# Kernel optimization log

Hardware: AMD Instinct MI355X
Metric: run time of the kernel (lower is better)

Reference implementation:

```python
import jax, jax.numpy as jnp
import numpy as np

H = 768
NH = 12
DH = H // NH  # 64
EPS = 1e-6


def _split_heads(x):
    # [B,S,H] -> [B,NH,S,DH]
    B, S, _ = x.shape
    return x.reshape(B, S, NH, DH).transpose(0, 2, 1, 3)


def setup_inputs() -> dict:
    key = jax.random.key(0)
    ks = jax.random.split(key, 16)
    B, S = 4, 1024
    sc = 0.02
    return {
        "hidden_states": jax.random.normal(ks[0], (B, S, H), jnp.float32),
        "time_embeddings": jax.random.normal(ks[1], (B, S, H), jnp.float32),
        "space_embeddings": jax.random.normal(ks[2], (B, S, H), jnp.float32),
        "attention_mask": jnp.zeros((B, 1, 1, S), jnp.float32),
        "Wq": jax.random.normal(ks[3], (H, H), jnp.float32) * sc,
        "bq": jnp.zeros((H,), jnp.float32),
        "Wk": jax.random.normal(ks[4], (H, H), jnp.float32) * sc,
        "bk": jnp.zeros((H,), jnp.float32),
        "Wv": jax.random.normal(ks[5], (H, H), jnp.float32) * sc,
        "bv": jnp.zeros((H,), jnp.float32),
        "Wt": jax.random.normal(ks[6], (H, H), jnp.float32) * sc,
        "bt": jnp.zeros((H,), jnp.float32),
        "Ws": jax.random.normal(ks[7], (H, H), jnp.float32) * sc,
        "bs": jnp.zeros((H,), jnp.float32),
    }


def reference(hidden_states, time_embeddings, space_embeddings, attention_mask,
              Wq, bq, Wk, bk, Wv, bv, Wt, bt, Ws, bs):
    q = _split_heads(hidden_states @ Wq.T + bq)   # [B,NH,S,DH]
    k = _split_heads(hidden_states @ Wk.T + bk)
    v = _split_heads(hidden_states @ Wv.T + bv)
    T = _split_heads(time_embeddings @ Wt.T + bt)
    Sp = _split_heads(space_embeddings @ Ws.T + bs)

    base = jnp.einsum("bhqd,bhkd->bhqk", q, k)
    T_norm = jnp.linalg.norm(T, axis=-1, keepdims=True)          # [B,NH,S,1]
    time_sim = jnp.einsum("bhqd,bhkd->bhqk", T, T) / (T_norm + EPS)
    S_norm = jnp.linalg.norm(Sp, axis=-1, keepdims=True)
    space_sim = jnp.einsum("bhqd,bhkd->bhqk", Sp, Sp) / (S_norm + EPS)

    scores = base * time_sim * space_sim / jnp.sqrt(jnp.float32(DH))
    scores = scores + attention_mask
    probs = jax.nn.softmax(scores, axis=-1)  # dropout is identity in eval
    ctx = jnp.einsum("bhqk,bhkd->bhqd", probs, v)
    B, _, S, _ = ctx.shape
    return ctx.transpose(0, 2, 1, 3).reshape(B, S, H)
```

## Files before the change

### kernel.cpp

```cpp
#include <hip/hip_runtime.h>

#define NHEADS 12
#define SEQ    1024
#define HDIM   768
#define DHEAD  64
#define BH_TOT 48
#define EPSN   1e-6f

typedef __attribute__((ext_vector_type(8))) short    bf8;
typedef __attribute__((ext_vector_type(4))) float    fx4;
typedef __attribute__((ext_vector_type(4))) _Float16 h4;

#define SZT 3145728u
#define WSZ 589824u

__device__ __forceinline__ float bf2f(unsigned short h) {
  union { unsigned int u; float f; } v; v.u = ((unsigned int)h) << 16; return v.f;
}
__device__ __forceinline__ unsigned short f2bf(float f) {
  union { float f; unsigned int u; } v; v.f = f;
  unsigned int u = v.u;
  return (unsigned short)((u + 0x7FFFu + ((u >> 16) & 1u)) >> 16);
}

typedef __attribute__((address_space(3))) unsigned int lds_u32;
typedef __attribute__((address_space(1))) const unsigned int glb_u32;
__device__ __forceinline__ void gld16(const unsigned short* g, unsigned short* l) {
  __builtin_amdgcn_global_load_lds((glb_u32*)g, (lds_u32*)l, 16, 0, 0);
}

__global__ void convert_kernel(const float* __restrict__ hs, const float* __restrict__ te,
                               const float* __restrict__ se,
                               const float* __restrict__ Wq, const float* __restrict__ Wk,
                               const float* __restrict__ Wv, const float* __restrict__ Wt,
                               const float* __restrict__ Ws2,
                               unsigned short* __restrict__ ws)
{
  const int z = blockIdx.y;
  const float* src;
  unsigned short* dst;
  int n;
  if (z < 3) {
    src = (z == 0) ? hs : (z == 1) ? te : se;
    dst = ws + (size_t)(5 + z) * SZT;
    n = 3145728;
  } else {
    src = (z == 3) ? Wq : (z == 4) ? Wk : (z == 5) ? Wv : (z == 6) ? Wt : Ws2;
    dst = ws + (size_t)8 * SZT + (size_t)(z - 3) * WSZ;
    n = 589824;
  }
  const int base = (blockIdx.x * 256 + threadIdx.x) * 8;
  if (base >= n) return;
  const fx4 a = *(const fx4*)(src + base);
  const fx4 b = *(const fx4*)(src + base + 4);
  bf8 o;
#pragma unroll
  for (int j = 0; j < 4; ++j) { o[j] = (short)f2bf(a[j]); o[4 + j] = (short)f2bf(b[j]); }
  *(bf8*)(dst + base) = o;
}

__global__ __launch_bounds__(256, 3)
void proj_kernel(unsigned short* __restrict__ ws,
                 const float* __restrict__ bq, const float* __restrict__ bk,
                 const float* __restrict__ bv, const float* __restrict__ bt,
                 const float* __restrict__ bs)
{
  __shared__ unsigned short Xs[2][4096];
  __shared__ unsigned short Ys[2][4096];

  const int z = blockIdx.z;
  const unsigned short* X = ws + (size_t)5 * SZT + (size_t)((z < 3) ? 0 : (z - 2)) * SZT;
  const unsigned short* W = ws + (size_t)8 * SZT + (size_t)z * WSZ;
  const float* bias = (z == 0) ? bq : (z == 1) ? bk : (z == 2) ? bv : (z == 3) ? bt : bs;
  unsigned short* out = ws + (size_t)((z < 2) ? z : (z == 2) ? 4 : (z == 3) ? 2 : 3) * SZT;

  const int tid   = threadIdx.x;
  const int lane  = tid & 63;
  const int wid   = tid >> 6;
  const int wm    = wid >> 1, wn = wid & 1;
  const int colid = lane & 15, quad = lane >> 4;
  const int m0 = blockIdx.y * 128, n0 = blockIdx.x * 128;

  auto stage = [&](int kt, int pb) {
#pragma unroll
    for (int i = 0; i < 2; ++i) {
      const int slot = i * 256 + tid;
      const int row = slot >> 2, ch = slot & 3;
      gld16(X + (m0 + row) * HDIM + kt + ch * 8, &Xs[pb][slot * 8]);
      gld16(W + (n0 + row) * HDIM + kt + ch * 8, &Ys[pb][slot * 8]);
    }
  };

  fx4 acc[4][4];
#pragma unroll
  for (int i = 0; i < 4; ++i)
#pragma unroll
    for (int j = 0; j < 4; ++j) acc[i][j] = (fx4){0.f, 0.f, 0.f, 0.f};

  stage(0, 0);
  __syncthreads();

  for (int it = 0; it < 24; ++it) {
    const int pb = it & 1;
    if (it + 1 < 24) stage((it + 1) * 32, pb ^ 1);

    bf8 af[4], bfr[4];
#pragma unroll
    for (int i = 0; i < 4; ++i)
      af[i] = *(const bf8*)&Xs[pb][(wm * 64 + i * 16 + colid) * 32 + quad * 8];
#pragma unroll
    for (int j = 0; j < 4; ++j)
      bfr[j] = *(const bf8*)&Ys[pb][(wn * 64 + j * 16 + colid) * 32 + quad * 8];
#pragma unroll
    for (int i = 0; i < 4; ++i)
#pragma unroll
      for (int j = 0; j < 4; ++j)
        acc[i][j] = __builtin_amdgcn_mfma_f32_16x16x32_bf16(af[i], bfr[j], acc[i][j], 0, 0, 0);
    __syncthreads();
  }

  if (z != 2) {
#pragma unroll
    for (int i = 0; i < 4; ++i) {
      const int r0 = m0 + wm * 64 + i * 16 + quad * 4;
      const int bb = r0 >> 10, s0 = r0 & 1023;
#pragma unroll
      for (int j = 0; j < 4; ++j) {
        const int c = n0 + wn * 64 + j * 16 + colid;
        const int h = c >> 6, d = c & 63;
        const float bvl = bias[c];
        unsigned short* op = out + (((bb * NHEADS + h) * SEQ + s0) * DHEAD + d);
#pragma unroll
        for (int reg = 0; reg < 4; ++reg)
          op[reg * DHEAD] = f2bf(acc[i][j][reg] + bvl);
      }
    }
  } else {
#pragma unroll
    for (int i = 0; i < 4; ++i) {
      const int r0 = m0 + wm * 64 + i * 16 + quad * 4;
      const int bb = r0 >> 10, s0 = r0 & 1023;
#pragma unroll
      for (int j = 0; j < 4; ++j) {
        const int c = n0 + wn * 64 + j * 16 + colid;
        const int h = c >> 6, d = c & 63;
        const float bvl = bias[c];
        h4 pk;
#pragma unroll
        for (int reg = 0; reg < 4; ++reg)
          pk[reg] = (_Float16)(acc[i][j][reg] + bvl);
        *(h4*)(void*)(out + ((size_t)((bb * NHEADS + h) * DHEAD + d)) * SEQ + s0) = pk;
      }
    }
  }
}

__global__ __launch_bounds__(256, 2)
void attn_kernel(const unsigned short* __restrict__ ws,
                 const float* __restrict__ maskb,
                 float* __restrict__ outb)
{
  const unsigned short* Qb  = ws;
  const unsigned short* GT0 = ws + (size_t)1 * SZT;
  const unsigned short* GT1 = ws + (size_t)2 * SZT;
  const unsigned short* GT2 = ws + (size_t)3 * SZT;
  const unsigned short* Vtu = ws + (size_t)4 * SZT;

  __shared__ unsigned short Ls[2][4][64][64];

  const int tid   = threadIdx.x;
  const int lane  = tid & 63;
  const int wid   = tid >> 6;
  const int colid = lane & 15, quad = lane >> 4;

  const int lin = blockIdx.x;
  const int xcd = lin & 7;
  const int idx = lin >> 3;
  const int bh  = xcd * 6 + (idx % 6);
  const int qx  = idx / 6;
  const int b   = bh / NHEADS, h = bh % NHEADS;
  const int q0  = qx * 128 + wid * 32;
  const int base_h = bh * SEQ * DHEAD;

  bf8 bqf[2][2], btf[2][2], bsf[2][2];
  float rs[2];
#pragma unroll
  for (int g = 0; g < 2; ++g) {
    const int row = q0 + g * 16 + colid;
    const unsigned short* qp = Qb  + base_h + row * 64 + quad * 8;
    const unsigned short* tp = GT1 + base_h + row * 64 + quad * 8;
    const unsigned short* sp = GT2 + base_h + row * 64 + quad * 8;
    bqf[g][0] = *(const bf8*)qp;  bqf[g][1] = *(const bf8*)(qp + 32);
    btf[g][0] = *(const bf8*)tp;  btf[g][1] = *(const bf8*)(tp + 32);
    bsf[g][0] = *(const bf8*)sp;  bsf[g][1] = *(const bf8*)(sp + 32);
    float t2 = 0.f, s2 = 0.f;
#pragma unroll
    for (int fr = 0; fr < 2; ++fr)
#pragma unroll
      for (int j = 0; j < 8; ++j) {
        const float tv = bf2f((unsigned short)btf[g][fr][j]);
        const float sv2 = bf2f((unsigned short)bsf[g][fr][j]);
        t2 += tv * tv; s2 += sv2 * sv2;
      }
    t2 += __shfl_xor(t2, 16); t2 += __shfl_xor(t2, 32);
    s2 += __shfl_xor(s2, 16); s2 += __shfl_xor(s2, 32);
    rs[g] = 1.0f / ((sqrtf(t2) + EPSN) * (sqrtf(s2) + EPSN) * 8.0f);
  }

  auto stage = [&](int kb, int pb) {
#pragma unroll
    for (int i = 0; i < 8; ++i) {
      const int s  = i * 256 + tid;
      const int r  = (s >> 3) & 63;
      const int cs = ((s & 7) ^ (r & 7)) * 8;
      unsigned short* dst = &Ls[pb][0][0][0] + s * 8;
      if (i < 2)      gld16(GT0 + base_h + (kb + r) * 64 + cs, dst);
      else if (i < 4) gld16(GT1 + base_h + (kb + r) * 64 + cs, dst);
      else if (i < 6) gld16(GT2 + base_h + (kb + r) * 64 + cs, dst);
      else            gld16(Vtu + ((size_t)(bh * 64 + r)) * 1024 + kb + cs, dst);
    }
  };

  float m_[2], l_[2];
  fx4 o[2][4];
#pragma unroll
  for (int g = 0; g < 2; ++g) {
    m_[g] = -1.0e30f; l_[g] = 0.f;
#pragma unroll
    for (int fd = 0; fd < 4; ++fd) o[g][fd] = (fx4){0.f, 0.f, 0.f, 0.f};
  }
  const fx4 zero = (fx4){0.f, 0.f, 0.f, 0.f};

  stage(0, 0);
  __syncthreads();

#pragma unroll 1
  for (int t = 0; t < 16; ++t) {
    const int pb = t & 1;
    if (t + 1 < 16) stage((t + 1) * 64, pb ^ 1);
    const int kb = t * 64;

#pragma unroll
    for (int hh = 0; hh < 2; ++hh) {
      bf8 ak[2][2], at_[2][2], as_[2][2];
      h4 vv[2][4];
      fx4 mk[2];
#pragma unroll
      for (int ff = 0; ff < 2; ++ff) {
        const int f   = hh * 2 + ff;
        const int row = f * 16 + colid;
        const int sw  = row & 7;
#pragma unroll
        for (int fr = 0; fr < 2; ++fr) {
          const int co = ((quad + fr * 4) ^ sw) * 8;
          ak[ff][fr]  = *(const bf8*)&Ls[pb][0][row][co];
          at_[ff][fr] = *(const bf8*)&Ls[pb][1][row][co];
          as_[ff][fr] = *(const bf8*)&Ls[pb][2][row][co];
        }
#pragma unroll
        for (int fd = 0; fd < 4; ++fd) {
          const int vr = fd * 16 + colid;
          const int vo = (((f * 2 + (quad >> 1)) ^ (vr & 7)) * 8) + (quad & 1) * 4;
          vv[ff][fd] = *(const h4*)&Ls[pb][3][vr][vo];
        }
        mk[ff] = *(const fx4*)(maskb + b * SEQ + kb + f * 16 + quad * 4);
      }

#pragma unroll
      for (int g = 0; g < 2; ++g) {
        float sv[2][4];
#pragma unroll
        for (int ff = 0; ff < 2; ++ff) {
          fx4 ab = __builtin_amdgcn_mfma_f32_16x16x32_bf16(ak[ff][0], bqf[g][0], zero, 0, 0, 0);
          ab = __builtin_amdgcn_mfma_f32_16x16x32_bf16(ak[ff][1], bqf[g][1], ab, 0, 0, 0);
          fx4 tt = __builtin_amdgcn_mfma_f32_16x16x32_bf16(at_[ff][0], btf[g][0], zero, 0, 0, 0);
          tt = __builtin_amdgcn_mfma_f32_16x16x32_bf16(at_[ff][1], btf[g][1], tt, 0, 0, 0);
          fx4 ss = __builtin_amdgcn_mfma_f32_16x16x32_bf16(as_[ff][0], bsf[g][0], zero, 0, 0, 0);
          ss = __builtin_amdgcn_mfma_f32_16x16x32_bf16(as_[ff][1], bsf[g][1], ss, 0, 0, 0);
#pragma unroll
          for (int reg = 0; reg < 4; ++reg)
            sv[ff][reg] = (ab[reg] * tt[reg]) * ss[reg] * rs[g] + mk[ff][reg];
        }

        float bm = sv[0][0];
#pragma unroll
        for (int ff = 0; ff < 2; ++ff)
#pragma unroll
          for (int reg = 0; reg < 4; ++reg) bm = fmaxf(bm, sv[ff][reg]);
        bm = fmaxf(bm, __shfl_xor(bm, 16));
        bm = fmaxf(bm, __shfl_xor(bm, 32));
        const float mn = fmaxf(m_[g], bm);
        const float alpha = __expf(m_[g] - mn);
        float rsum = 0.f;
        h4 pa[2];
#pragma unroll
        for (int ff = 0; ff < 2; ++ff)
#pragma unroll
          for (int reg = 0; reg < 4; ++reg) {
            const float p = __expf(sv[ff][reg] - mn);
            rsum += p;
            pa[ff][reg] = (_Float16)p;
          }
        rsum += __shfl_xor(rsum, 16);
        rsum += __shfl_xor(rsum, 32);
        l_[g] = l_[g] * alpha + rsum;
        m_[g] = mn;

        float ar[4];
#pragma unroll
        for (int reg = 0; reg < 4; ++reg) ar[reg] = __shfl(alpha, quad * 4 + reg);
#pragma unroll
        for (int fd = 0; fd < 4; ++fd)
#pragma unroll
          for (int reg = 0; reg < 4; ++reg) o[g][fd][reg] *= ar[reg];

#pragma unroll
        for (int ff = 0; ff < 2; ++ff)
#pragma unroll
          for (int fd = 0; fd < 4; ++fd)
            o[g][fd] = __builtin_amdgcn_mfma_f32_16x16x16f16(pa[ff], vv[ff][fd], o[g][fd], 0, 0, 0);
      }
    }
    __syncthreads();
  }

#pragma unroll
  for (int g = 0; g < 2; ++g) {
    const float linv = 1.0f / l_[g];
    float ir[4];
#pragma unroll
    for (int reg = 0; reg < 4; ++reg) ir[reg] = __shfl(linv, quad * 4 + reg);
#pragma unroll
    for (int reg = 0; reg < 4; ++reg) {
      const int s = q0 + g * 16 + quad * 4 + reg;
#pragma unroll
      for (int fd = 0; fd < 4; ++fd)
        outb[(size_t)(b * SEQ + s) * HDIM + h * DHEAD + fd * 16 + colid] = o[g][fd][reg] * ir[reg];
    }
  }
}

extern "C" void kernel_launch(void* const* d_in, const int* in_sizes, int n_in,
                              void* d_out, int out_size, void* d_ws, size_t ws_size,
                              hipStream_t stream)
{
  (void)in_sizes; (void)n_in; (void)out_size; (void)ws_size;
  const float* hs   = (const float*)d_in[0];
  const float* te   = (const float*)d_in[1];
  const float* se   = (const float*)d_in[2];
  const float* mask = (const float*)d_in[3];
  const float* Wq   = (const float*)d_in[4];
  const float* bq   = (const float*)d_in[5];
  const float* Wk   = (const float*)d_in[6];
  const float* bk   = (const float*)d_in[7];
  const float* Wv   = (const float*)d_in[8];
  const float* bv   = (const float*)d_in[9];
  const float* Wt   = (const float*)d_in[10];
  const float* bt   = (const float*)d_in[11];
  const float* Wsp  = (const float*)d_in[12];
  const float* bsp  = (const float*)d_in[13];
  float* out = (float*)d_out;
  unsigned short* ws = (unsigned short*)d_ws;

  convert_kernel<<<dim3(1536, 8), 256, 0, stream>>>(hs, te, se, Wq, Wk, Wv, Wt, Wsp, ws);
  proj_kernel<<<dim3(6, 32, 5), 256, 0, stream>>>(ws, bq, bk, bv, bt, bsp);
  attn_kernel<<<dim3(384), 256, 0, stream>>>(ws, mask, out);
}
```

Before: 202.7 us.

## Halve query rows per block, double grid, read V directly from global

The attention kernel now processes 16 query rows per wave (64 per block) instead of 32, so the grid doubles to 768 blocks. V is no longer staged through LDS; each wave loads its V fragments straight from global memory, which shrinks shared memory to three K/T/S tiles and raises the launch-bounds occupancy target to 3 blocks per CU. The goal is better CU fill and more latency hiding. The cost is that each K/T/S tile staged in LDS is reused by half as many query rows, and the uncached global V reads add latency inside the inner loop.

```diff
diff --git a/kernel.cpp b/kernel.cpp
--- a/kernel.cpp
+++ b/kernel.cpp
@@ -155,7 +155,7 @@
   }
 }
 
-__global__ __launch_bounds__(256, 2)
+__global__ __launch_bounds__(256, 3)
 void attn_kernel(const unsigned short* __restrict__ ws,
                  const float* __restrict__ maskb,
                  float* __restrict__ outb)
@@ -164,9 +164,9 @@
   const unsigned short* GT0 = ws + (size_t)1 * SZT;
   const unsigned short* GT1 = ws + (size_t)2 * SZT;
   const unsigned short* GT2 = ws + (size_t)3 * SZT;
-  const unsigned short* Vtu = ws + (size_t)4 * SZT;
-
-  __shared__ unsigned short Ls[2][4][64][64];
+  const _Float16* Vtf = (const _Float16*)(ws + (size_t)4 * SZT);
+
+  __shared__ unsigned short Ls[2][3][64][64];
 
   const int tid   = threadIdx.x;
   const int lane  = tid & 63;
@@ -179,56 +179,50 @@
   const int bh  = xcd * 6 + (idx % 6);
   const int qx  = idx / 6;
   const int b   = bh / NHEADS, h = bh % NHEADS;
-  const int q0  = qx * 128 + wid * 32;
+  const int q0  = qx * 64 + wid * 16;
   const int base_h = bh * SEQ * DHEAD;
 
-  bf8 bqf[2][2], btf[2][2], bsf[2][2];
-  float rs[2];
-#pragma unroll
-  for (int g = 0; g < 2; ++g) {
-    const int row = q0 + g * 16 + colid;
+  bf8 bqf[2], btf[2], bsf[2];
+  float rs;
+  {
+    const int row = q0 + colid;
     const unsigned short* qp = Qb  + base_h + row * 64 + quad * 8;
     const unsigned short* tp = GT1 + base_h + row * 64 + quad * 8;
     const unsigned short* sp = GT2 + base_h + row * 64 + quad * 8;
-    bqf[g][0] = *(const bf8*)qp;  bqf[g][1] = *(const bf8*)(qp + 32);
-    btf[g][0] = *(const bf8*)tp;  btf[g][1] = *(const bf8*)(tp + 32);
-    bsf[g][0] = *(const bf8*)sp;  bsf[g][1] = *(const bf8*)(sp + 32);
+    bqf[0] = *(const bf8*)qp;  bqf[1] = *(const bf8*)(qp + 32);
+    btf[0] = *(const bf8*)tp;  btf[1] = *(const bf8*)(tp + 32);
+    bsf[0] = *(const bf8*)sp;  bsf[1] = *(const bf8*)(sp + 32);
     float t2 = 0.f, s2 = 0.f;
 #pragma unroll
     for (int fr = 0; fr < 2; ++fr)
 #pragma unroll
       for (int j = 0; j < 8; ++j) {
-        const float tv = bf2f((unsigned short)btf[g][fr][j]);
-        const float sv2 = bf2f((unsigned short)bsf[g][fr][j]);
+        const float tv = bf2f((unsigned short)btf[fr][j]);
+        const float sv2 = bf2f((unsigned short)bsf[fr][j]);
         t2 += tv * tv; s2 += sv2 * sv2;
       }
     t2 += __shfl_xor(t2, 16); t2 += __shfl_xor(t2, 32);
     s2 += __shfl_xor(s2, 16); s2 += __shfl_xor(s2, 32);
-    rs[g] = 1.0f / ((sqrtf(t2) + EPSN) * (sqrtf(s2) + EPSN) * 8.0f);
+    rs = 1.0f / ((sqrtf(t2) + EPSN) * (sqrtf(s2) + EPSN) * 8.0f);
   }
 
   auto stage = [&](int kb, int pb) {
 #pragma unroll
-    for (int i = 0; i < 8; ++i) {
+    for (int i = 0; i < 6; ++i) {
       const int s  = i * 256 + tid;
       const int r  = (s >> 3) & 63;
       const int cs = ((s & 7) ^ (r & 7)) * 8;
       unsigned short* dst = &Ls[pb][0][0][0] + s * 8;
       if (i < 2)      gld16(GT0 + base_h + (kb + r) * 64 + cs, dst);
       else if (i < 4) gld16(GT1 + base_h + (kb + r) * 64 + cs, dst);
-      else if (i < 6) gld16(GT2 + base_h + (kb + r) * 64 + cs, dst);
-      else            gld16(Vtu + ((size_t)(bh * 64 + r)) * 1024 + kb + cs, dst);
+      else            gld16(GT2 + base_h + (kb + r) * 64 + cs, dst);
     }
   };
 
-  float m_[2], l_[2];
-  fx4 o[2][4];
-#pragma unroll
-  for (int g = 0; g < 2; ++g) {
-    m_[g] = -1.0e30f; l_[g] = 0.f;
-#pragma unroll
-    for (int fd = 0; fd < 4; ++fd) o[g][fd] = (fx4){0.f, 0.f, 0.f, 0.f};
-  }
+  float m_ = -1.0e30f, l_ = 0.f;
+  fx4 o[4];
+#pragma unroll
+  for (int fd = 0; fd < 4; ++fd) o[fd] = (fx4){0.f, 0.f, 0.f, 0.f};
   const fx4 zero = (fx4){0.f, 0.f, 0.f, 0.f};
 
   stage(0, 0);
@@ -258,84 +252,78 @@
           as_[ff][fr] = *(const bf8*)&Ls[pb][2][row][co];
         }
 #pragma unroll
-        for (int fd = 0; fd < 4; ++fd) {
-          const int vr = fd * 16 + colid;
-          const int vo = (((f * 2 + (quad >> 1)) ^ (vr & 7)) * 8) + (quad & 1) * 4;
-          vv[ff][fd] = *(const h4*)&Ls[pb][3][vr][vo];
+        for (int fd = 0; fd < 4; ++fd)
+          vv[ff][fd] = *(const h4*)(Vtf + (size_t)(bh * DHEAD + fd * 16 + colid) * SEQ
+                                        + kb + f * 16 + quad * 4);
+        mk[ff] = *(const fx4*)(maskb + b * SEQ + kb + f * 16 + quad * 4);
+      }
+
+      float sv[2][4];
+#pragma unroll
+      for (int ff = 0; ff < 2; ++ff) {
+        fx4 ab = __builtin_amdgcn_mfma_f32_16x16x32_bf16(ak[ff][0], bqf[0], zero, 0, 0, 0);
+        ab = __builtin_amdgcn_mfma_f32_16x16x32_bf16(ak[ff][1], bqf[1], ab, 0, 0, 0);
+        fx4 tt = __builtin_amdgcn_mfma_f32_16x16x32_bf16(at_[ff][0], btf[0], zero, 0, 0, 0);
+        tt = __builtin_amdgcn_mfma_f32_16x16x32_bf16(at_[ff][1], btf[1], tt, 0, 0, 0);
+        fx4 ss = __builtin_amdgcn_mfma_f32_16x16x32_bf16(as_[ff][0], bsf[0], zero, 0, 0, 0);
+        ss = __builtin_amdgcn_mfma_f32_16x16x32_bf16(as_[ff][1], bsf[1], ss, 0, 0, 0);
+#pragma unroll
+        for (int reg = 0; reg < 4; ++reg)
+          sv[ff][reg] = (ab[reg] * tt[reg]) * ss[reg] * rs + mk[ff][reg];
+      }
+
+      float bm = sv[0][0];
+#pragma unroll
+      for (int ff = 0; ff < 2; ++ff)
+#pragma unroll
+        for (int reg = 0; reg < 4; ++reg) bm = fmaxf(bm, sv[ff][reg]);
+      bm = fmaxf(bm, __shfl_xor(bm, 16));
+      bm = fmaxf(bm, __shfl_xor(bm, 32));
+      const float mn = fmaxf(m_, bm);
+      const float alpha = __expf(m_ - mn);
+      float rsum = 0.f;
+      h4 pa[2];
+#pragma unroll
+      for (int ff = 0; ff < 2; ++ff)
+#pragma unroll
+        for (int reg = 0; reg < 4; ++reg) {
+          const float p = __expf(sv[ff][reg] - mn);
+          rsum += p;
+          pa[ff][reg] = (_Float16)p;
         }
-        mk[ff] = *(const fx4*)(maskb + b * SEQ + kb + f * 16 + quad * 4);
-      }
-
-#pragma unroll
-      for (int g = 0; g < 2; ++g) {
-        float sv[2][4];
-#pragma unroll
-        for (int ff = 0; ff < 2; ++ff) {
-          fx4 ab = __builtin_amdgcn_mfma_f32_16x16x32_bf16(ak[ff][0], bqf[g][0], zero, 0, 0, 0);
-          ab = __builtin_amdgcn_mfma_f32_16x16x32_bf16(ak[ff][1], bqf[g][1], ab, 0, 0, 0);
-          fx4 tt = __builtin_amdgcn_mfma_f32_16x16x32_bf16(at_[ff][0], btf[g][0], zero, 0, 0, 0);
-          tt = __builtin_amdgcn_mfma_f32_16x16x32_bf16(at_[ff][1], btf[g][1], tt, 0, 0, 0);
-          fx4 ss = __builtin_amdgcn_mfma_f32_16x16x32_bf16(as_[ff][0], bsf[g][0], zero, 0, 0, 0);
-          ss = __builtin_amdgcn_mfma_f32_16x16x32_bf16(as_[ff][1], bsf[g][1], ss, 0, 0, 0);
-#pragma unroll
-          for (int reg = 0; reg < 4; ++reg)
-            sv[ff][reg] = (ab[reg] * tt[reg]) * ss[reg] * rs[g] + mk[ff][reg];
-        }
-
-        float bm = sv[0][0];
-#pragma unroll
-        for (int ff = 0; ff < 2; ++ff)
-#pragma unroll
-          for (int reg = 0; reg < 4; ++reg) bm = fmaxf(bm, sv[ff][reg]);
-        bm = fmaxf(bm, __shfl_xor(bm, 16));
-        bm = fmaxf(bm, __shfl_xor(bm, 32));
-        const float mn = fmaxf(m_[g], bm);
-        const float alpha = __expf(m_[g] - mn);
-        float rsum = 0.f;
-        h4 pa[2];
-#pragma unroll
-        for (int ff = 0; ff < 2; ++ff)
-#pragma unroll
-          for (int reg = 0; reg < 4; ++reg) {
-            const float p = __expf(sv[ff][reg] - mn);
-            rsum += p;
-            pa[ff][reg] = (_Float16)p;
-          }
-        rsum += __shfl_xor(rsum, 16);
-        rsum += __shfl_xor(rsum, 32);
-        l_[g] = l_[g] * alpha + rsum;
-        m_[g] = mn;
-
-        float ar[4];
-#pragma unroll
-        for (int reg = 0; reg < 4; ++reg) ar[reg] = __shfl(alpha, quad * 4 + reg);
+      rsum += __shfl_xor(rsum, 16);
+      rsum += __shfl_xor(rsum, 32);
+      l_ = l_ * alpha + rsum;
+      m_ = mn;
+
+      float ar[4];
+#pragma unroll
+      for (int reg = 0; reg < 4; ++reg) ar[reg] = __shfl(alpha, quad * 4 + reg);
+#pragma unroll
+      for (int fd = 0; fd < 4; ++fd)
+#pragma unroll
+        for (int reg = 0; reg < 4; ++reg) o[fd][reg] *= ar[reg];
+
+#pragma unroll
+      for (int ff = 0; ff < 2; ++ff)
 #pragma unroll
         for (int fd = 0; fd < 4; ++fd)
-#pragma unroll
-          for (int reg = 0; reg < 4; ++reg) o[g][fd][reg] *= ar[reg];
-
-#pragma unroll
-        for (int ff = 0; ff < 2; ++ff)
-#pragma unroll
-          for (int fd = 0; fd < 4; ++fd)
-            o[g][fd] = __builtin_amdgcn_mfma_f32_16x16x16f16(pa[ff], vv[ff][fd], o[g][fd], 0, 0, 0);
-      }
+          o[fd] = __builtin_amdgcn_mfma_f32_16x16x16f16(pa[ff], vv[ff][fd], o[fd], 0, 0, 0);
     }
     __syncthreads();
   }
 
-#pragma unroll
-  for (int g = 0; g < 2; ++g) {
-    const float linv = 1.0f / l_[g];
+  {
+    const float linv = 1.0f / l_;
     float ir[4];
 #pragma unroll
     for (int reg = 0; reg < 4; ++reg) ir[reg] = __shfl(linv, quad * 4 + reg);
 #pragma unroll
     for (int reg = 0; reg < 4; ++reg) {
-      const int s = q0 + g * 16 + quad * 4 + reg;
+      const int s = q0 + quad * 4 + reg;
 #pragma unroll
       for (int fd = 0; fd < 4; ++fd)
-        outb[(size_t)(b * SEQ + s) * HDIM + h * DHEAD + fd * 16 + colid] = o[g][fd][reg] * ir[reg];
+        outb[(size_t)(b * SEQ + s) * HDIM + h * DHEAD + fd * 16 + colid] = o[fd][reg] * ir[reg];
     }
   }
 }
@@ -364,5 +352,5 @@
 
   convert_kernel<<<dim3(1536, 8), 256, 0, stream>>>(hs, te, se, Wq, Wk, Wv, Wt, Wsp, ws);
   proj_kernel<<<dim3(6, 32, 5), 256, 0, stream>>>(ws, bq, bk, bv, bt, bsp);
-  attn_kernel<<<dim3(384), 256, 0, stream>>>(ws, mask, out);
-}
+  attn_kernel<<<dim3(768), 256, 0, stream>>>(ws, mask, out);
+}
```

Measured after the change: 252.1 us. +24.4%, slower.
